# Kernel optimization log

Measured on AMD Instinct MI355X. Metric: run time of the kernel, lower is better.

## Reference

```python
import jax, jax.numpy as jnp
import numpy as np

N_RAYS = 262144  # 512x512 image
N_PTS = 64       # hardcoded in original forward (reshape(-1, 64, 3))
FAR_DELTA = 1e10 # sentinel delta appended for the last sample


def setup_inputs() -> dict:
    key = jax.random.key(0)
    k1, k2, k3 = jax.random.split(key, 3)
    # non-negative densities, as a density field would produce
    density = jax.random.uniform(k1, (N_RAYS, N_PTS, 1), dtype=jnp.float32)
    # sorted depths along each ray in [2, 6] (typical near/far bounds)
    depth_values = jnp.sort(
        2.0 + 4.0 * jax.random.uniform(k2, (N_RAYS, N_PTS), dtype=jnp.float32),
        axis=-1,
    )
    rays_feature = jax.random.uniform(k3, (N_RAYS, N_PTS, 3), dtype=jnp.float32)
    return {"density": density, "depth_values": depth_values, "rays_feature": rays_feature}


def reference(density, depth_values, rays_feature):
    # deltas: consecutive depth differences, with huge sentinel for last sample
    deltas = jnp.concatenate(
        [depth_values[:, 1:] - depth_values[:, :-1],
         jnp.full_like(depth_values[:, :1], FAR_DELTA)],
        axis=-1,
    )  # (N, P)
    sigma_delta = density[..., 0] * deltas          # (N, P)
    trans_step = jnp.exp(-sigma_delta)              # per-segment transmittance e
    # exclusive cumulative product: T_0 = 1, T_i = prod_{j<i} e_j
    transmittance = jnp.concatenate(
        [jnp.ones_like(trans_step[:, :1]),
         jnp.cumprod(trans_step[:, :-1], axis=1)],
        axis=1,
    )  # (N, P)
    weights = transmittance * (1.0 - trans_step)    # (N, P)
    feature = jnp.sum(weights[..., None] * rays_feature, axis=1)  # (N, 3)
    depth = jnp.sum(weights * depth_values, axis=1)               # (N,)
    return feature, depth
```

## Files before the change

kernel.cpp:

```cpp
#include <hip/hip_runtime.h>
#include <hip/hip_bf16.h>

#define N_RAYS 262144
#define N_PTS  64
#define FAR_DELTA 1e10f

#define RPB 64
#define ST  16
#define NT  (N_PTS/ST)

#define DS_STRIDE 17
#define FT_STRIDE 49

__global__ __launch_bounds__(64) void volume_render_kernel(
    const float* __restrict__ density,
    const float* __restrict__ depth_values,
    const float* __restrict__ rays_feature,
    float* __restrict__ out)
{
    __shared__ float s_dens[RPB * DS_STRIDE];
    __shared__ float s_dep [RPB * DS_STRIDE];
    __shared__ float s_feat[RPB * FT_STRIDE];

    const int t    = threadIdx.x;
    const int ray0 = blockIdx.x * RPB;

    float T = 1.0f;
    float ax = 0.f, ay = 0.f, az = 0.f, ad = 0.f;
    float sig_p = 0.f, d_p = 0.f, fx_p = 0.f, fy_p = 0.f, fz_p = 0.f;

    #pragma unroll
    for (int tile = 0; tile < NT; ++tile) {
        const int s0 = tile * ST;
        __syncthreads();

        #pragma unroll
        for (int i = 0; i < 4; ++i) {
            const unsigned flat = i * 64u + t;
            const int r = flat >> 2;
            const int q = flat & 3;
            const size_t g = (size_t)(ray0 + r) * N_PTS + s0 + q * 4;
            const float4 dv = *(const float4*)(density + g);
            const float4 zv = *(const float4*)(depth_values + g);
            float* dd = &s_dens[r * DS_STRIDE + q * 4];
            float* zz = &s_dep [r * DS_STRIDE + q * 4];
            dd[0] = dv.x; dd[1] = dv.y; dd[2] = dv.z; dd[3] = dv.w;
            zz[0] = zv.x; zz[1] = zv.y; zz[2] = zv.z; zz[3] = zv.w;
        }
        #pragma unroll
        for (int i = 0; i < 12; ++i) {
            const unsigned flat = i * 64u + t;
            const unsigned r = flat / 12u;
            const unsigned q = flat - r * 12u;
            const size_t g = (size_t)(ray0 + r) * (N_PTS * 3) + s0 * 3 + q * 4;
            const float4 fv = *(const float4*)(rays_feature + g);
            float* ff = &s_feat[r * FT_STRIDE + q * 4];
            ff[0] = fv.x; ff[1] = fv.y; ff[2] = fv.z; ff[3] = fv.w;
        }
        __syncthreads();

        #pragma unroll
        for (int j = 0; j < ST; ++j) {
            const float d  = s_dep [t * DS_STRIDE + j];
            const float sg = s_dens[t * DS_STRIDE + j];
            const float fx = s_feat[t * FT_STRIDE + 3 * j + 0];
            const float fy = s_feat[t * FT_STRIDE + 3 * j + 1];
            const float fz = s_feat[t * FT_STRIDE + 3 * j + 2];
            if (tile > 0 || j > 0) {
                const float delta = d - d_p;
                const float e = __expf(-sig_p * delta);
                const float w = T * (1.0f - e);
                ax += w * fx_p; ay += w * fy_p; az += w * fz_p; ad += w * d_p;
                T *= e;
            }
            sig_p = sg; d_p = d; fx_p = fx; fy_p = fy; fz_p = fz;
        }
    }

    {
        const float e = __expf(-sig_p * FAR_DELTA);
        const float w = T * (1.0f - e);
        ax += w * fx_p; ay += w * fy_p; az += w * fz_p; ad += w * d_p;
    }

    const int ray = ray0 + t;
    out[(size_t)ray * 3 + 0] = ax;
    out[(size_t)ray * 3 + 1] = ay;
    out[(size_t)ray * 3 + 2] = az;
    out[(size_t)N_RAYS * 3 + ray] = ad;
}

extern "C" void kernel_launch(void* const* d_in, const int* in_sizes, int n_in,
                              void* d_out, int out_size, void* d_ws, size_t ws_size,
                              hipStream_t stream) {
    const float* density      = (const float*)d_in[0];
    const float* depth_values = (const float*)d_in[1];
    const float* rays_feature = (const float*)d_in[2];
    float* out = (float*)d_out;

    const int blocks = N_RAYS / RPB;
    volume_render_kernel<<<blocks, RPB, 0, stream>>>(
        density, depth_values, rays_feature, out);
}
```

Before: 365.9 us.

## Halve sample tile, vectorize LDS access, and drop barriers in single-wave blocks

Shrinks the per-tile sample count from 16 to 8 and repads the shared-memory rows to 16-byte-aligned strides. This lowers shared memory per block so more waves can be resident, and it allows float4 LDS stores and loads in both the staging and consume phases. The __syncthreads calls are removed on the basis that a 64-thread block is a single wavefront. It also adds a minimum-blocks launch-bounds hint. The risks are more tiles per ray, some bank conflicts from the new strides, and reliance on wavefront lockstep instead of explicit barriers.

```diff
diff --git a/kernel.cpp b/kernel.cpp
--- a/kernel.cpp
+++ b/kernel.cpp
@@ -6,13 +6,13 @@
 #define FAR_DELTA 1e10f
 
 #define RPB 64
-#define ST  16
+#define ST  8
 #define NT  (N_PTS/ST)
 
-#define DS_STRIDE 17
-#define FT_STRIDE 49
+#define DS_STRIDE 12
+#define FT_STRIDE 28
 
-__global__ __launch_bounds__(64) void volume_render_kernel(
+__global__ __launch_bounds__(64, 3) void volume_render_kernel(
     const float* __restrict__ density,
     const float* __restrict__ depth_values,
     const float* __restrict__ rays_feature,
@@ -32,48 +32,53 @@
     #pragma unroll
     for (int tile = 0; tile < NT; ++tile) {
         const int s0 = tile * ST;
-        __syncthreads();
 
         #pragma unroll
-        for (int i = 0; i < 4; ++i) {
-            const unsigned flat = i * 64u + t;
-            const int r = flat >> 2;
-            const int q = flat & 3;
+        for (int i = 0; i < 2; ++i) {
+            const int flat = i * 64 + t;
+            const int r = flat >> 1;
+            const int q = flat & 1;
             const size_t g = (size_t)(ray0 + r) * N_PTS + s0 + q * 4;
             const float4 dv = *(const float4*)(density + g);
             const float4 zv = *(const float4*)(depth_values + g);
-            float* dd = &s_dens[r * DS_STRIDE + q * 4];
-            float* zz = &s_dep [r * DS_STRIDE + q * 4];
-            dd[0] = dv.x; dd[1] = dv.y; dd[2] = dv.z; dd[3] = dv.w;
-            zz[0] = zv.x; zz[1] = zv.y; zz[2] = zv.z; zz[3] = zv.w;
+            *(float4*)&s_dens[r * DS_STRIDE + q * 4] = dv;
+            *(float4*)&s_dep [r * DS_STRIDE + q * 4] = zv;
         }
         #pragma unroll
-        for (int i = 0; i < 12; ++i) {
-            const unsigned flat = i * 64u + t;
-            const unsigned r = flat / 12u;
-            const unsigned q = flat - r * 12u;
+        for (int i = 0; i < 6; ++i) {
+            const int flat = i * 64 + t;
+            const int r = flat / 6;
+            const int q = flat - r * 6;
             const size_t g = (size_t)(ray0 + r) * (N_PTS * 3) + s0 * 3 + q * 4;
-            const float4 fv = *(const float4*)(rays_feature + g);
-            float* ff = &s_feat[r * FT_STRIDE + q * 4];
-            ff[0] = fv.x; ff[1] = fv.y; ff[2] = fv.z; ff[3] = fv.w;
+            *(float4*)&s_feat[r * FT_STRIDE + q * 4] = *(const float4*)(rays_feature + g);
         }
-        __syncthreads();
 
         #pragma unroll
-        for (int j = 0; j < ST; ++j) {
-            const float d  = s_dep [t * DS_STRIDE + j];
-            const float sg = s_dens[t * DS_STRIDE + j];
-            const float fx = s_feat[t * FT_STRIDE + 3 * j + 0];
-            const float fy = s_feat[t * FT_STRIDE + 3 * j + 1];
-            const float fz = s_feat[t * FT_STRIDE + 3 * j + 2];
-            if (tile > 0 || j > 0) {
-                const float delta = d - d_p;
-                const float e = __expf(-sig_p * delta);
-                const float w = T * (1.0f - e);
-                ax += w * fx_p; ay += w * fy_p; az += w * fz_p; ad += w * d_p;
-                T *= e;
+        for (int jj = 0; jj < 2; ++jj) {
+            const float4 dq = *(const float4*)&s_dep [t * DS_STRIDE + jj * 4];
+            const float4 sq = *(const float4*)&s_dens[t * DS_STRIDE + jj * 4];
+            const float4 f0 = *(const float4*)&s_feat[t * FT_STRIDE + jj * 12 + 0];
+            const float4 f1 = *(const float4*)&s_feat[t * FT_STRIDE + jj * 12 + 4];
+            const float4 f2 = *(const float4*)&s_feat[t * FT_STRIDE + jj * 12 + 8];
+
+            const float d [4] = {dq.x, dq.y, dq.z, dq.w};
+            const float sg[4] = {sq.x, sq.y, sq.z, sq.w};
+            const float fx[4] = {f0.x, f0.w, f1.z, f2.y};
+            const float fy[4] = {f0.y, f1.x, f1.w, f2.z};
+            const float fz[4] = {f0.z, f1.y, f2.x, f2.w};
+
+            #pragma unroll
+            for (int s = 0; s < 4; ++s) {
+                if (tile > 0 || jj > 0 || s > 0) {
+                    const float delta = d[s] - d_p;
+                    const float e = __expf(-sig_p * delta);
+                    const float w = T * (1.0f - e);
+                    ax += w * fx_p; ay += w * fy_p; az += w * fz_p; ad += w * d_p;
+                    T *= e;
+                }
+                sig_p = sg[s]; d_p = d[s];
+                fx_p = fx[s]; fy_p = fy[s]; fz_p = fz[s];
             }
-            sig_p = sg; d_p = d; fx_p = fx; fy_p = fy; fz_p = fz;
         }
     }
 
```

Result: slower. 379.8 us (+3.8%).
